# Performance work log

Hardware: AMD Instinct MI355X
Metric: run time of the kernel (lower is better)

## Reference

```python
import jax, jax.numpy as jnp
import numpy as np

DILATIONS = (1, 3, 5)
NUM_HEADS = 2


def _conv(x, w, b, dil=1, pad=0):
    # x: [B,C,H,W], w: [O,I,kh,kw] (OIHW), 'same'-style padding = dilation for k=3
    y = jax.lax.conv_general_dilated(
        x, w, window_strides=(1, 1), padding=[(pad, pad), (pad, pad)],
        rhs_dilation=(dil, dil), dimension_numbers=('NCHW', 'OIHW', 'NCHW'))
    return y + b[None, :, None, None]


def setup_inputs() -> dict:
    key = jax.random.key(0)
    ks = jax.random.split(key, 4)
    B, Cin, H, W = 4, 256, 64, 64
    Cout = 256
    x = jax.random.normal(ks[0], (B, Cin, H, W), dtype=jnp.float32)
    # kaiming-uniform-like init scale
    q_w = jax.random.uniform(ks[1], (Cout, Cin, 3, 3), dtype=jnp.float32,
                             minval=-1.0, maxval=1.0) * np.sqrt(6.0 / (Cin * 9))
    k_w = jax.random.uniform(ks[2], (Cout, Cin, 1, 1), dtype=jnp.float32,
                             minval=-1.0, maxval=1.0) * np.sqrt(6.0 / Cin)
    v_w = jax.random.uniform(ks[3], (Cout, Cin, 1, 1), dtype=jnp.float32,
                             minval=-1.0, maxval=1.0) * np.sqrt(6.0 / Cin)
    q_b = jnp.zeros((Cout,), jnp.float32)
    k_b = jnp.zeros((Cout,), jnp.float32)
    v_b = jnp.zeros((Cout,), jnp.float32)
    return {"x": x, "q_w": q_w, "q_b": q_b, "k_w": k_w, "k_b": k_b,
            "v_w": v_w, "v_b": v_b}


def reference(x, q_w, q_b, k_w, k_b, v_w, v_b):
    B, C, H, W = x.shape
    Cout = q_w.shape[0]
    hd = Cout // NUM_HEADS  # head_dim
    # ds_conv2d: sum of SiLU(dilated conv) over dilations 1,3,5 (padding=dilation)
    q = sum(jax.nn.silu(_conv(x, q_w, q_b, dil=d, pad=d)) for d in DILATIONS)
    k = _conv(x, k_w, k_b)
    v = _conv(x, v_w, v_b)
    N = H * W
    # [B, heads, head_dim, N]
    q = q.reshape(B, NUM_HEADS, hd, N)
    k = k.reshape(B, NUM_HEADS, hd, N)
    v = v.reshape(B, NUM_HEADS, hd, N)
    # energy[b,h,n,m] = sum_d q[b,h,d,n] * k[b,h,d,m]
    energy = jnp.einsum('bhdn,bhdm->bhnm', q, k)
    attn = jax.nn.softmax(energy / jnp.sqrt(jnp.float32(hd)), axis=-1)
    # out[b,h,n,d] = sum_m attn[b,h,n,m] * v[b,h,d,m]; then back to [B,C,H,W]
    out = jnp.einsum('bhnm,bhdm->bhdn', attn, v)
    return out.reshape(B, Cout, H, W)
```

## Files before the change

### kernel.cpp

```cpp
#include <hip/hip_runtime.h>
#include <cstdint>

typedef __attribute__((ext_vector_type(8))) _Float16 f16x8;
typedef __attribute__((ext_vector_type(4))) float f32x4;

#define DEV static __device__ __forceinline__

DEV void gld_lds16(void* lds_base, const void* gsrc) {
  __builtin_amdgcn_global_load_lds(
      (const __attribute__((address_space(1))) unsigned int*)gsrc,
      (__attribute__((address_space(3))) unsigned int*)lds_base,
      16, 0, 0);
}
DEV unsigned short f2h(float f) {
  _Float16 h = (_Float16)f;
  return __builtin_bit_cast(unsigned short, h);
}
DEV float h2f(unsigned short u) {
  _Float16 h = __builtin_bit_cast(_Float16, u);
  return (float)h;
}
DEV unsigned pk2h(float a, float b) {
  auto h2 = __builtin_amdgcn_cvt_pkrtz(a, b);
  return __builtin_bit_cast(unsigned, h2);
}
DEV float v_exp2(float x) { float r; asm("v_exp_f32 %0, %1" : "=v"(r) : "v"(x)); return r; }
DEV float v_rcp(float x) { float r; asm("v_rcp_f32 %0, %1" : "=v"(r) : "v"(x)); return r; }


__global__ __launch_bounds__(256) void k_prep_x(
    const float* __restrict__ x, char* __restrict__ xpad,
    const float* __restrict__ qw, const float* __restrict__ kw, const float* __restrict__ vw,
    unsigned short* __restrict__ Wq, unsigned short* __restrict__ Wk, unsigned short* __restrict__ Wv) {
  __shared__ float xs[32 * 257];
  int h = blockIdx.x, b = blockIdx.y, t = threadIdx.x;
  int gid = (b * 64 + h) * 256 + t;
  const float* q9 = qw + (size_t)gid * 9;
#pragma unroll
  for (int tp = 0; tp < 9; tp++) Wq[tp * 65536 + gid] = f2h(q9[tp]);
  Wk[gid] = f2h(kw[gid]);
  Wv[gid] = f2h(vw[gid]);
  uint4 z = {0, 0, 0, 0};
  char* rowbase = xpad + ((size_t)(b * 74 + h + 5) * 74) * 512;
  for (int i = t; i < 320; i += 256) {
    int col = i >> 5, off = (i & 31) * 16;
    int w = (col < 5) ? col : 64 + col;
    *(uint4*)(rowbase + (size_t)w * 512 + off) = z;
  }
  if (h < 10) {
    int r = (h < 5) ? h : 64 + h;
    char* rb = xpad + ((size_t)(b * 74 + r) * 74) * 512;
    for (int i = t; i < 2368; i += 256) *(uint4*)(rb + (size_t)i * 16) = z;
  }
  const float* xb = x + (size_t)b * 1048576 + h * 64;
  for (int half = 0; half < 2; half++) {
    int w0 = half * 32;
    for (int kk = 0; kk < 32; kk++) {
      int flat = kk * 256 + t;
      int ci = flat >> 5, w = flat & 31;
      xs[w * 257 + ci] = xb[ci * 4096 + w0 + w];
    }
    __syncthreads();
    for (int g = 0; g < 4; g++) {
      int w = g * 8 + (t >> 5);
      int cg = t & 31;
      float v0 = xs[w * 257 + cg * 8 + 0], v1 = xs[w * 257 + cg * 8 + 1];
      float v2 = xs[w * 257 + cg * 8 + 2], v3 = xs[w * 257 + cg * 8 + 3];
      float v4 = xs[w * 257 + cg * 8 + 4], v5 = xs[w * 257 + cg * 8 + 5];
      float v6 = xs[w * 257 + cg * 8 + 6], v7 = xs[w * 257 + cg * 8 + 7];
      uint4 pk;
      pk.x = pk2h(v0, v1);
      pk.y = pk2h(v2, v3);
      pk.z = pk2h(v4, v5);
      pk.w = pk2h(v6, v7);
      *(uint4*)(xpad + ((size_t)((b * 74 + h + 5) * 74) + w0 + w + 5) * 512 + cg * 16) = pk;
    }
    __syncthreads();
  }
}

__global__ __launch_bounds__(256, 2) void k_conv_kv(
    const char* __restrict__ xpad, const unsigned short* __restrict__ Wk,
    const unsigned short* __restrict__ Wv, const float* __restrict__ kb,
    const float* __restrict__ vb, unsigned short* __restrict__ K, unsigned short* __restrict__ V) {
  __shared__ char sm[65536];
  int t = threadIdx.x, lane = t & 63, wid = t >> 6, q4 = lane >> 4, l15 = lane & 15;
  int px0 = blockIdx.x * 128;
  int b = px0 >> 12, nn = px0 & 4095;
  int h = blockIdx.y;
  int mode = blockIdx.z;
  int co0 = h * 128;
  const char* Wsrc = (const char*)(mode ? Wv : Wk);
  int wm = wid & 1, wn = wid >> 1;

#define STAGE_KV(base_, c_)                                                       \
  {                                                                               \
    for (int ch = wid * 1024; ch < 16384; ch += 4096) {                           \
      int o = ch + lane * 16;                                                     \
      int r = o >> 7;                                                             \
      int n = nn + r, hh = n >> 6, ww2 = n & 63;                                  \
      int col = (o & 127) ^ ((r & 7) << 4);                                       \
      gld_lds16((base_) + ch,                                                     \
                xpad + ((size_t)((b * 74 + hh + 5) * 74) + ww2 + 5) * 512 + (c_)*128 + col); \
    }                                                                             \
    for (int ch = wid * 1024; ch < 16384; ch += 4096) {                           \
      int o = ch + lane * 16;                                                     \
      int r = o >> 7;                                                             \
      int col = (o & 127) ^ ((r & 7) << 4);                                       \
      gld_lds16((base_) + 16384 + ch, Wsrc + (co0 + r) * 512 + (c_)*128 + col);   \
    }                                                                             \
  }

  STAGE_KV(sm, 0);
  asm volatile("s_waitcnt vmcnt(0)" ::: "memory");
  __syncthreads();

  f32x4 acc[4][4] = {};
  for (int c = 0; c < 4; c++) {
    char* cb = sm + (c & 1) * 32768;
    if (c < 3) STAGE_KV(sm + ((c & 1) ^ 1) * 32768, c + 1);
    const char* Xs = cb;
    const char* Ws = cb + 16384;
    int xg = mode ? wn : wm;
    int wg = mode ? wm : wn;
#pragma unroll
    for (int kt = 0; kt < 2; kt++) {
      f16x8 xf[4], wf[4];
#pragma unroll
      for (int i = 0; i < 4; i++) {
        int rx = xg * 64 + i * 16 + l15;
        xf[i] = *(const f16x8*)(Xs + ((rx * 128 + kt * 64 + q4 * 16) ^ ((rx & 7) << 4)));
        int rw = wg * 64 + i * 16 + l15;
        wf[i] = *(const f16x8*)(Ws + ((rw * 128 + kt * 64 + q4 * 16) ^ ((rw & 7) << 4)));
      }
#pragma unroll
      for (int m = 0; m < 4; m++)
#pragma unroll
        for (int n = 0; n < 4; n++)
          acc[m][n] = mode ? __builtin_amdgcn_mfma_f32_16x16x32_f16(wf[m], xf[n], acc[m][n], 0, 0, 0)
                           : __builtin_amdgcn_mfma_f32_16x16x32_f16(xf[m], wf[n], acc[m][n], 0, 0, 0);
    }
    asm volatile("s_waitcnt vmcnt(0)" ::: "memory");
    __syncthreads();
  }
#undef STAGE_KV
  int bh = b * 2 + h;
  if (mode == 0) {
#pragma unroll
    for (int m = 0; m < 4; m++)
#pragma unroll
      for (int n = 0; n < 4; n++) {
        int dd = wn * 64 + n * 16 + l15;
        float bias = kb[co0 + dd];
#pragma unroll
        for (int j = 0; j < 4; j++) {
          int npix = nn + wm * 64 + m * 16 + q4 * 4 + j;
          K[(size_t)(bh * 4096 + npix) * 128 + dd] = f2h(acc[m][n][j] + bias);
        }
      }
  } else {
#pragma unroll
    for (int m = 0; m < 4; m++)
#pragma unroll
      for (int j = 0; j < 4; j++) {
        int cr = wm * 64 + m * 16 + q4 * 4 + j;
        float bias = vb[co0 + cr];
#pragma unroll
        for (int n = 0; n < 4; n++) {
          int pc = nn + wn * 64 + (n >> 1) * 32 + (l15 >> 2) * 8 + (n & 1) * 4 + (l15 & 3);
          V[(size_t)(bh * 128 + cr) * 4096 + pc] = f2h(acc[m][n][j] + bias);
        }
      }
  }
}

__global__ __launch_bounds__(512, 2) void k_conv_q(
    const char* __restrict__ xpad, const unsigned short* __restrict__ Wq,
    const float* __restrict__ qb, unsigned short* __restrict__ Q) {
  extern __shared__ char sm[];
  int t = threadIdx.x, lane = t & 63, wid = t >> 6, q4 = lane >> 4, l15 = lane & 15;
  int fblk = blockIdx.x;
  int g = (fblk & 7) * 32 + (fblk >> 3);
  int h2 = g & 31, b = (g >> 5) & 3, ch2 = g >> 7;
  int h0 = h2 * 2;
  int co0 = ch2 * 128;
  int wn = wid & 1, wq = wid >> 1;
  int hr = wq >> 1, wloc = wq & 1;
  const int dil[3] = {1, 3, 5};
  const char* WqB = (const char*)Wq;
  f32x4 accd[3][2][4] = {};

#define STAGE_B(dstbuf, kh_, c_, kw_)                                             \
  {                                                                               \
    const char* src_ = WqB + (size_t)((kh_)*3 + (kw_)) * 131072 + co0 * 512 + (c_)*128; \
    char* dst_ = (dstbuf);                                                        \
    for (int ch = wid * 1024; ch < 16384; ch += 8192) {                           \
      int o = ch + lane * 16;                                                     \
      int r = o >> 7;                                                             \
      int col = (o & 127) ^ ((r & 7) << 4);                                       \
      gld_lds16(dst_ + ch, src_ + r * 512 + col);                                 \
    }                                                                             \
  }

#define STAGE_A_ROW(abase_, slot_, pr_, c_)                                       \
  {                                                                               \
    const char* src_ = xpad + ((size_t)(b * 74 + (pr_)) * 74) * 512 + (c_)*128;   \
    char* dst_ = (abase_) + (slot_)*9472;                                         \
    for (int ch = wid * 1024; ch < 9472; ch += 8192) {                            \
      int o = ch + lane * 16;                                                     \
      if (o < 9472) {                                                             \
        int r = o >> 7;                                                           \
        int col = (o & 127) ^ ((r & 7) << 4);                                     \
        gld_lds16(dst_ + ch, src_ + r * 512 + col);                               \
      }                                                                           \
    }                                                                             \
  }

#define STAGE_A(abase_, kh_, c_)                                                  \
  {                                                                               \
    if ((kh_) == 1) {                                                             \
      for (int s = 0; s < 2; s++) STAGE_A_ROW(abase_, s, h0 + s + 5, c_);         \
    } else {                                                                      \
      for (int di = 0; di < 3; di++)                                              \
        for (int s = 0; s < 2; s++)                                               \
          STAGE_A_ROW(abase_, di * 2 + s, h0 + s + ((kh_)-1) * dil[di] + 5, c_);  \
    }                                                                             \
  }

  STAGE_A(sm + 32768, 0, 0);
  STAGE_B(sm, 0, 0, 0);
  asm volatile("s_waitcnt vmcnt(0)" ::: "memory");
  __syncthreads();

  int curB = 0, curA = 0;
  for (int kh = 0; kh < 3; kh++) {
    for (int c = 0; c < 4; c++) {
      int cn2 = c + 1, khn2 = kh;
      if (cn2 == 4) { cn2 = 0; khn2 = kh + 1; }
      for (int kw = 0; kw < 3; kw++) {
        int kwn = kw + 1, cn = c, khn = kh;
        if (kwn == 3) { kwn = 0; cn = c + 1; if (cn == 4) { cn = 0; khn = kh + 1; } }
        char* Bnext = curB ? sm : sm + 16384;
        if (khn < 3) STAGE_B(Bnext, khn, cn, kwn);
        if (kw == 0 && khn2 < 3) STAGE_A(sm + 32768 + (curA ^ 1) * 56832, khn2, cn2);
        const char* Bc = curB ? sm + 16384 : sm;
        const char* Abase = sm + 32768 + curA * 56832;
        f16x8 bf[4][2];
#pragma unroll
        for (int n = 0; n < 4; n++)
#pragma unroll
          for (int kt = 0; kt < 2; kt++) {
            int rc = wn * 64 + n * 16 + l15;
            bf[n][kt] = *(const f16x8*)(Bc + ((rc * 128 + kt * 64 + q4 * 16) ^ ((rc & 7) << 4)));
          }
#pragma unroll
        for (int di = 0; di < 3; di++) {
          int dw = (kw - 1) * dil[di] + 5;
          const char* Ad = Abase + (kh == 1 ? hr : di * 2 + hr) * 9472;
          f16x8 af[2][2];
#pragma unroll
          for (int m = 0; m < 2; m++)
#pragma unroll
            for (int kt = 0; kt < 2; kt++) {
              int wp = wloc * 32 + m * 16 + l15 + dw;
              af[m][kt] = *(const f16x8*)(Ad + ((wp * 128 + kt * 64 + q4 * 16) ^ ((wp & 7) << 4)));
            }
          __builtin_amdgcn_s_setprio(1);
#pragma unroll
          for (int m = 0; m < 2; m++)
#pragma unroll
            for (int n = 0; n < 4; n++)
#pragma unroll
              for (int kt = 0; kt < 2; kt++)
                accd[di][m][n] = __builtin_amdgcn_mfma_f32_16x16x32_f16(af[m][kt], bf[n][kt], accd[di][m][n], 0, 0, 0);
          __builtin_amdgcn_s_setprio(0);
        }
        asm volatile("s_waitcnt vmcnt(0)" ::: "memory");
        __syncthreads();
        curB ^= 1;
      }
      if (khn2 < 3) curA ^= 1;
    }
  }
#undef STAGE_A
#undef STAGE_A_ROW
#undef STAGE_B
  const float LOG2E = 1.4426950408889634f;
  const float QSCALE = 0.12751879523176862f;
#pragma unroll
  for (int n = 0; n < 4; n++) {
    float bias = qb[co0 + wn * 64 + n * 16 + l15];
#pragma unroll
    for (int m = 0; m < 2; m++)
#pragma unroll
      for (int j = 0; j < 4; j++) {
        float s = 0.f;
#pragma unroll
        for (int di = 0; di < 3; di++) {
          float v = accd[di][m][n][j] + bias;
          s += v * v_rcp(1.0f + v_exp2(-v * LOG2E));
        }
        int w = wloc * 32 + m * 16 + q4 * 4 + j;
        int npix = (h0 + hr) * 64 + w;
        int dd = wn * 64 + n * 16 + l15;
        Q[((size_t)(b * 2 + ch2) * 4096 + npix) * 128 + dd] = f2h(s * QSCALE);
      }
  }
}

__global__ __launch_bounds__(256, 2) void k_attn(
    const unsigned short* __restrict__ Q, const unsigned short* __restrict__ K,
    const unsigned short* __restrict__ V, float* __restrict__ out,
    unsigned short* __restrict__ o1buf, float* __restrict__ mlbuf) {
  __shared__ char sm[65536];
  int t = threadIdx.x, lane = t & 63, wid = t >> 6, q4 = lane >> 4, l15 = lane & 15;
  int fblk = blockIdx.x;
  int g = (fblk & 7) * 64 + (fblk >> 3);
  int nb = g & 31, bh = (g >> 5) & 7, half = g >> 8;
  int b = bh >> 1, hh = bh & 1;
  int n0 = nb * 128;
  const char* Qg = (const char*)(Q + ((size_t)bh * 4096 + n0) * 128);
  const char* Kg = (const char*)(K + (size_t)bh * 4096 * 128) + half * 524288;
  const char* Vg = (const char*)(V + (size_t)bh * 128 * 4096) + half * 4096;
  f16x8 qf[2][4];
#pragma unroll
  for (int nt = 0; nt < 2; nt++)
#pragma unroll
    for (int kt = 0; kt < 4; kt++) {
      int rn = wid * 32 + nt * 16 + l15;
      qf[nt][kt] = *(const f16x8*)(Qg + (size_t)rn * 256 + kt * 64 + q4 * 16);
    }
  const char* pT0 = sm + (((l15 * 256 + 0 * 64 + q4 * 16) ^ (l15 << 4)));
  const char* pT1 = sm + (((l15 * 256 + 1 * 64 + q4 * 16) ^ (l15 << 4)));
  const char* pT2 = sm + (((l15 * 256 + 2 * 64 + q4 * 16) ^ (l15 << 4)));
  const char* pT3 = sm + (((l15 * 256 + 3 * 64 + q4 * 16) ^ (l15 << 4)));
  const char* pU0 = sm + 32768 + (((l15 * 128 + 0 * 64 + q4 * 16) ^ ((l15 & 7) << 4)));
  const char* pU1 = sm + 32768 + (((l15 * 128 + 1 * 64 + q4 * 16) ^ ((l15 & 7) << 4)));
  int ks[4], vs[4], lch[4];
#pragma unroll
  for (int c2 = 0; c2 < 4; c2++) {
    int ch = wid * 1024 + c2 * 4096;
    int o = ch + lane * 16;
    lch[c2] = ch;
    ks[c2] = o ^ (((o >> 8) & 15) << 4);
    int dd = o >> 7;
    vs[c2] = dd * 8192 + ((o & 127) ^ ((dd & 7) << 4));
  }
#pragma unroll
  for (int c2 = 0; c2 < 4; c2++) gld_lds16(sm + lch[c2], Kg + ks[c2]);
#pragma unroll
  for (int c2 = 0; c2 < 4; c2++) gld_lds16(sm + 32768 + lch[c2], Vg + vs[c2]);
  asm volatile("s_waitcnt vmcnt(0)" ::: "memory");
  __syncthreads();
  f32x4 Ofr[8][2] = {};
  float mrun[2] = {-3e38f, -3e38f};
  float lrun[2] = {0.f, 0.f};
  const char* kgp = Kg;
  const char* vgp = Vg;

#define ATTN_ITER(KB, VB, KBN, VBN, do_pf)                                          \
  {                                                                                 \
    if (do_pf) {                                                                    \
      kgp += 16384;                                                                 \
      vgp += 128;                                                                   \
      _Pragma("unroll") for (int c2 = 0; c2 < 4; c2++)                              \
          gld_lds16(sm + (KBN) + lch[c2], kgp + ks[c2]);                            \
      _Pragma("unroll") for (int c2 = 0; c2 < 4; c2++)                              \
          gld_lds16(sm + (VBN) + lch[c2], vgp + vs[c2]);                            \
    }                                                                               \
    f32x4 sT[4][2] = {};                                                            \
    _Pragma("unroll") for (int kt = 0; kt < 4; kt++) {                              \
      const char* pT = (kt == 0) ? pT0 : (kt == 1) ? pT1 : (kt == 2) ? pT2 : pT3;   \
      f16x8 kf[4];                                                                  \
      _Pragma("unroll") for (int mt = 0; mt < 4; mt++)                              \
          kf[mt] = *(const f16x8*)(pT + (KB) + mt * 4096);                          \
      __builtin_amdgcn_s_setprio(1);                                                \
      _Pragma("unroll") for (int mt = 0; mt < 4; mt++)                              \
          _Pragma("unroll") for (int nt = 0; nt < 2; nt++)                          \
              sT[mt][nt] = __builtin_amdgcn_mfma_f32_16x16x32_f16(                  \
                  kf[mt], qf[nt][kt], sT[mt][nt], 0, 0, 0);                         \
      __builtin_amdgcn_s_setprio(0);                                                \
    }                                                                               \
    unsigned U[2][4][2];                                                            \
    _Pragma("unroll") for (int nt = 0; nt < 2; nt++) {                              \
      float mx = sT[0][nt][0];                                                      \
      _Pragma("unroll") for (int mt = 0; mt < 4; mt++)                              \
          _Pragma("unroll") for (int j = 0; j < 4; j++) mx = fmaxf(mx, sT[mt][nt][j]); \
      mx = fmaxf(mx, __shfl_xor(mx, 16));                                           \
      mx = fmaxf(mx, __shfl_xor(mx, 32));                                           \
      float mn = mrun[nt];                                                          \
      if (!__all(mx - mn <= 8.f)) {                                                 \
        mn = fmaxf(mrun[nt], mx);                                                   \
        float al = v_exp2(mrun[nt] - mn);                                           \
        mrun[nt] = mn;                                                              \
        lrun[nt] *= al;                                                             \
        _Pragma("unroll") for (int dt = 0; dt < 8; dt++) Ofr[dt][nt] *= al;         \
      }                                                                             \
      float rs = 0.f;                                                               \
      _Pragma("unroll") for (int mt = 0; mt < 4; mt++) {                            \
        float p0 = v_exp2(sT[mt][nt][0] - mn);                                      \
        float p1 = v_exp2(sT[mt][nt][1] - mn);                                      \
        float p2 = v_exp2(sT[mt][nt][2] - mn);                                      \
        float p3 = v_exp2(sT[mt][nt][3] - mn);                                      \
        rs += (p0 + p1) + (p2 + p3);                                                \
        U[nt][mt][0] = pk2h(p0, p1);                                                \
        U[nt][mt][1] = pk2h(p2, p3);                                                \
      }                                                                             \
      rs += __shfl_xor(rs, 16);                                                     \
      rs += __shfl_xor(rs, 32);                                                     \
      lrun[nt] += rs;                                                               \
    }                                                                               \
    _Pragma("unroll") for (int kt = 0; kt < 2; kt++) {                              \
      const char* pU = kt ? pU1 : pU0;                                              \
      f16x8 pf[2];                                                                  \
      _Pragma("unroll") for (int nt = 0; nt < 2; nt++) {                            \
        uint4 fr;                                                                   \
        fr.x = U[nt][2 * kt][0];                                                    \
        fr.y = U[nt][2 * kt][1];                                                    \
        fr.z = U[nt][2 * kt + 1][0];                                                \
        fr.w = U[nt][2 * kt + 1][1];                                                \
        pf[nt] = __builtin_bit_cast(f16x8, fr);                                     \
      }                                                                             \
      f16x8 vf[8];                                                                  \
      _Pragma("unroll") for (int dt = 0; dt < 8; dt++)                              \
          vf[dt] = *(const f16x8*)(pU + ((VB)-32768) + dt * 2048);                  \
      __builtin_amdgcn_s_setprio(1);                                                \
      _Pragma("unroll") for (int dt = 0; dt < 8; dt++)                              \
          _Pragma("unroll") for (int nt = 0; nt < 2; nt++)                          \
              Ofr[dt][nt] = __builtin_amdgcn_mfma_f32_16x16x32_f16(                 \
                  vf[dt], pf[nt], Ofr[dt][nt], 0, 0, 0);                            \
      __builtin_amdgcn_s_setprio(0);                                                \
    }                                                                               \
    __syncthreads();                                                                \
  }

  for (int it2 = 0; it2 < 16; it2++) {
    ATTN_ITER(0, 32768, 16384, 49152, true);
    ATTN_ITER(16384, 49152, 0, 32768, (it2 < 15));
  }
#undef ATTN_ITER

  if (q4 == 0) {
#pragma unroll
    for (int nt = 0; nt < 2; nt++) {
      int n = n0 + wid * 32 + nt * 16 + l15;
      float2 ml;
      ml.x = mrun[nt];
      ml.y = lrun[nt];
      *(float2*)(mlbuf + ((size_t)(half * 8 + bh) * 4096 + n) * 2) = ml;
    }
  }
  if (half == 0) {
    float* og = out + (size_t)(b * 256 + hh * 128) * 4096 + n0 + wid * 32;
#pragma unroll
    for (int dt = 0; dt < 8; dt++)
#pragma unroll
      for (int nt = 0; nt < 2; nt++)
#pragma unroll
        for (int j = 0; j < 4; j++) {
          int dd = dt * 16 + q4 * 4 + j;
          og[(size_t)dd * 4096 + nt * 16 + l15] = Ofr[dt][nt][j];
        }
  } else {
    float li[2] = {v_rcp(lrun[0]), v_rcp(lrun[1])};
    unsigned short* og = o1buf + (size_t)bh * 128 * 4096 + n0 + wid * 32;
#pragma unroll
    for (int dt = 0; dt < 8; dt++)
#pragma unroll
      for (int nt = 0; nt < 2; nt++)
#pragma unroll
        for (int j = 0; j < 4; j++) {
          int dd = dt * 16 + q4 * 4 + j;
          og[(size_t)dd * 4096 + nt * 16 + l15] = f2h(Ofr[dt][nt][j] * li[nt]);
        }
  }
}

__global__ __launch_bounds__(256) void k_combine(
    float* __restrict__ out, const unsigned short* __restrict__ o1,
    const float* __restrict__ ml) {
  int tid = blockIdx.x * 256 + threadIdx.x;
  int n = tid & 4095, dg = (tid >> 12) & 7, bh = tid >> 15;
  float2 ml0 = *(const float2*)(ml + ((size_t)bh * 4096 + n) * 2);
  float2 ml1 = *(const float2*)(ml + ((size_t)(8 + bh) * 4096 + n) * 2);
  float ms = fmaxf(ml0.x, ml1.x);
  float a0 = v_exp2(ml0.x - ms);
  float w1 = ml1.y * v_exp2(ml1.x - ms);
  float inv = 1.f / (ml0.y * a0 + w1);
  size_t ob = ((size_t)((bh >> 1) * 256 + (bh & 1) * 128 + dg * 16)) * 4096 + n;
  size_t o1b = ((size_t)(bh * 128 + dg * 16)) * 4096 + n;
#pragma unroll 4
  for (int j = 0; j < 16; j++) {
    float v0 = out[ob + (size_t)j * 4096];
    float v1 = h2f(o1[o1b + (size_t)j * 4096]);
    out[ob + (size_t)j * 4096] = (v0 * a0 + v1 * w1) * inv;
  }
}

extern "C" void kernel_launch(void* const* d_in, const int* in_sizes, int n_in,
                              void* d_out, int out_size, void* d_ws, size_t ws_size,
                              hipStream_t stream) {
  (void)in_sizes; (void)n_in; (void)out_size;
  const float* x  = (const float*)d_in[0];
  const float* qw = (const float*)d_in[1];
  const float* qb = (const float*)d_in[2];
  const float* kw = (const float*)d_in[3];
  const float* kb = (const float*)d_in[4];
  const float* vw = (const float*)d_in[5];
  const float* vb = (const float*)d_in[6];
  char* ws = (char*)d_ws;
  if (ws_size < 37822464) return;
  char* xpad = ws;
  unsigned short* Wq = (unsigned short*)(ws + 11214848);
  unsigned short* Wk = (unsigned short*)(ws + 12394496);
  unsigned short* Wv = (unsigned short*)(ws + 12525568);
  unsigned short* Qb = (unsigned short*)(ws + 12656640);
  unsigned short* Kb = (unsigned short*)(ws + 21045248);
  unsigned short* Vb = (unsigned short*)(ws + 29433856);
  unsigned short* O1 = (unsigned short*)ws;
  float* ML = (float*)(ws + 11214848);
  k_prep_x<<<dim3(64, 4), dim3(256), 0, stream>>>(x, xpad, qw, kw, vw, Wq, Wk, Wv);
  k_conv_kv<<<dim3(128, 2, 2), dim3(256), 0, stream>>>(xpad, Wk, Wv, kb, vb, Kb, Vb);
  k_conv_q<<<dim3(256), dim3(512), 146432, stream>>>(xpad, Wq, qb, Qb);
  k_attn<<<dim3(512), dim3(256), 0, stream>>>(Qb, Kb, Vb, (float*)d_out, O1, ML);
  k_combine<<<dim3(1024), dim3(256), 0, stream>>>((float*)d_out, O1, ML);
}
```

Baseline: 164.2 us.

## Merge split-KV halves into one block and combine partial softmax in LDS

The attention kernel now runs both KV halves as two 256-thread groups inside one 512-thread block, each with its own 64KB LDS region. Group 1 passes its unnormalized accumulators and running max/sum to group 0 through LDS, and group 0 merges them and writes the final output. This removes the separate combine kernel, the fp16 partial-output and max/sum buffers, and the extra read-modify-write of the fp32 output in global memory. In exchange it uses 128KB of dynamic LDS per block, adds a block-wide barrier plus an LDS exchange at the end, and leaves half the threads idle during the final store.

```diff
diff --git a/kernel.cpp b/kernel.cpp
--- a/kernel.cpp
+++ b/kernel.cpp
@@ -15,10 +15,6 @@
 DEV unsigned short f2h(float f) {
   _Float16 h = (_Float16)f;
   return __builtin_bit_cast(unsigned short, h);
-}
-DEV float h2f(unsigned short u) {
-  _Float16 h = __builtin_bit_cast(_Float16, u);
-  return (float)h;
 }
 DEV unsigned pk2h(float a, float b) {
   auto h2 = __builtin_amdgcn_cvt_pkrtz(a, b);
@@ -308,17 +304,18 @@
   }
 }
 
-__global__ __launch_bounds__(256, 2) void k_attn(
+__global__ __launch_bounds__(512) void k_attn(
     const unsigned short* __restrict__ Q, const unsigned short* __restrict__ K,
-    const unsigned short* __restrict__ V, float* __restrict__ out,
-    unsigned short* __restrict__ o1buf, float* __restrict__ mlbuf) {
-  __shared__ char sm[65536];
+    const unsigned short* __restrict__ V, float* __restrict__ out) {
+  extern __shared__ char sm[];
   int t = threadIdx.x, lane = t & 63, wid = t >> 6, q4 = lane >> 4, l15 = lane & 15;
+  int half = wid >> 2, wv = wid & 3;
   int fblk = blockIdx.x;
-  int g = (fblk & 7) * 64 + (fblk >> 3);
-  int nb = g & 31, bh = (g >> 5) & 7, half = g >> 8;
+  int g = (fblk & 7) * 32 + (fblk >> 3);
+  int nb = g & 31, bh = g >> 5;
   int b = bh >> 1, hh = bh & 1;
   int n0 = nb * 128;
+  char* smg = sm + half * 65536;
   const char* Qg = (const char*)(Q + ((size_t)bh * 4096 + n0) * 128);
   const char* Kg = (const char*)(K + (size_t)bh * 4096 * 128) + half * 524288;
   const char* Vg = (const char*)(V + (size_t)bh * 128 * 4096) + half * 4096;
@@ -327,19 +324,19 @@
   for (int nt = 0; nt < 2; nt++)
 #pragma unroll
     for (int kt = 0; kt < 4; kt++) {
-      int rn = wid * 32 + nt * 16 + l15;
+      int rn = wv * 32 + nt * 16 + l15;
       qf[nt][kt] = *(const f16x8*)(Qg + (size_t)rn * 256 + kt * 64 + q4 * 16);
     }
-  const char* pT0 = sm + (((l15 * 256 + 0 * 64 + q4 * 16) ^ (l15 << 4)));
-  const char* pT1 = sm + (((l15 * 256 + 1 * 64 + q4 * 16) ^ (l15 << 4)));
-  const char* pT2 = sm + (((l15 * 256 + 2 * 64 + q4 * 16) ^ (l15 << 4)));
-  const char* pT3 = sm + (((l15 * 256 + 3 * 64 + q4 * 16) ^ (l15 << 4)));
-  const char* pU0 = sm + 32768 + (((l15 * 128 + 0 * 64 + q4 * 16) ^ ((l15 & 7) << 4)));
-  const char* pU1 = sm + 32768 + (((l15 * 128 + 1 * 64 + q4 * 16) ^ ((l15 & 7) << 4)));
+  const char* pT0 = smg + (((l15 * 256 + 0 * 64 + q4 * 16) ^ (l15 << 4)));
+  const char* pT1 = smg + (((l15 * 256 + 1 * 64 + q4 * 16) ^ (l15 << 4)));
+  const char* pT2 = smg + (((l15 * 256 + 2 * 64 + q4 * 16) ^ (l15 << 4)));
+  const char* pT3 = smg + (((l15 * 256 + 3 * 64 + q4 * 16) ^ (l15 << 4)));
+  const char* pU0 = smg + 32768 + (((l15 * 128 + 0 * 64 + q4 * 16) ^ ((l15 & 7) << 4)));
+  const char* pU1 = smg + 32768 + (((l15 * 128 + 1 * 64 + q4 * 16) ^ ((l15 & 7) << 4)));
   int ks[4], vs[4], lch[4];
 #pragma unroll
   for (int c2 = 0; c2 < 4; c2++) {
-    int ch = wid * 1024 + c2 * 4096;
+    int ch = wv * 1024 + c2 * 4096;
     int o = ch + lane * 16;
     lch[c2] = ch;
     ks[c2] = o ^ (((o >> 8) & 15) << 4);
@@ -347,9 +344,9 @@
     vs[c2] = dd * 8192 + ((o & 127) ^ ((dd & 7) << 4));
   }
 #pragma unroll
-  for (int c2 = 0; c2 < 4; c2++) gld_lds16(sm + lch[c2], Kg + ks[c2]);
-#pragma unroll
-  for (int c2 = 0; c2 < 4; c2++) gld_lds16(sm + 32768 + lch[c2], Vg + vs[c2]);
+  for (int c2 = 0; c2 < 4; c2++) gld_lds16(smg + lch[c2], Kg + ks[c2]);
+#pragma unroll
+  for (int c2 = 0; c2 < 4; c2++) gld_lds16(smg + 32768 + lch[c2], Vg + vs[c2]);
   asm volatile("s_waitcnt vmcnt(0)" ::: "memory");
   __syncthreads();
   f32x4 Ofr[8][2] = {};
@@ -364,9 +361,9 @@
       kgp += 16384;                                                                 \
       vgp += 128;                                                                   \
       _Pragma("unroll") for (int c2 = 0; c2 < 4; c2++)                              \
-          gld_lds16(sm + (KBN) + lch[c2], kgp + ks[c2]);                            \
+          gld_lds16(smg + (KBN) + lch[c2], kgp + ks[c2]);                           \
       _Pragma("unroll") for (int c2 = 0; c2 < 4; c2++)                              \
-          gld_lds16(sm + (VBN) + lch[c2], vgp + vs[c2]);                            \
+          gld_lds16(smg + (VBN) + lch[c2], vgp + vs[c2]);                           \
     }                                                                               \
     f32x4 sT[4][2] = {};                                                            \
     _Pragma("unroll") for (int kt = 0; kt < 4; kt++) {                              \
@@ -440,18 +437,35 @@
   }
 #undef ATTN_ITER
 
-  if (q4 == 0) {
+  float* xch = (float*)sm;
+  float* mlx = (float*)(sm + 65536);
+  int slot = t & 255;
+  if (half == 1) {
+#pragma unroll
+    for (int dt = 0; dt < 8; dt++)
+#pragma unroll
+      for (int nt = 0; nt < 2; nt++)
+#pragma unroll
+        for (int j = 0; j < 4; j++)
+          xch[(dt * 8 + nt * 4 + j) * 256 + slot] = Ofr[dt][nt][j];
+    mlx[slot] = mrun[0];
+    mlx[256 + slot] = mrun[1];
+    mlx[512 + slot] = lrun[0];
+    mlx[768 + slot] = lrun[1];
+  }
+  __syncthreads();
+  if (half == 0) {
+    float m1[2] = {mlx[slot], mlx[256 + slot]};
+    float l1[2] = {mlx[512 + slot], mlx[768 + slot]};
+    float a0[2], a1[2], li[2];
 #pragma unroll
     for (int nt = 0; nt < 2; nt++) {
-      int n = n0 + wid * 32 + nt * 16 + l15;
-      float2 ml;
-      ml.x = mrun[nt];
-      ml.y = lrun[nt];
-      *(float2*)(mlbuf + ((size_t)(half * 8 + bh) * 4096 + n) * 2) = ml;
+      float ms = fmaxf(mrun[nt], m1[nt]);
+      a0[nt] = v_exp2(mrun[nt] - ms);
+      a1[nt] = v_exp2(m1[nt] - ms);
+      li[nt] = v_rcp(lrun[nt] * a0[nt] + l1[nt] * a1[nt]);
     }
-  }
-  if (half == 0) {
-    float* og = out + (size_t)(b * 256 + hh * 128) * 4096 + n0 + wid * 32;
+    float* og = out + (size_t)(b * 256 + hh * 128) * 4096 + n0 + wv * 32;
 #pragma unroll
     for (int dt = 0; dt < 8; dt++)
 #pragma unroll
@@ -459,41 +473,10 @@
 #pragma unroll
         for (int j = 0; j < 4; j++) {
           int dd = dt * 16 + q4 * 4 + j;
-          og[(size_t)dd * 4096 + nt * 16 + l15] = Ofr[dt][nt][j];
+          float o1v = xch[(dt * 8 + nt * 4 + j) * 256 + slot];
+          og[(size_t)dd * 4096 + nt * 16 + l15] =
+              (Ofr[dt][nt][j] * a0[nt] + o1v * a1[nt]) * li[nt];
         }
-  } else {
-    float li[2] = {v_rcp(lrun[0]), v_rcp(lrun[1])};
-    unsigned short* og = o1buf + (size_t)bh * 128 * 4096 + n0 + wid * 32;
-#pragma unroll
-    for (int dt = 0; dt < 8; dt++)
-#pragma unroll
-      for (int nt = 0; nt < 2; nt++)
-#pragma unroll
-        for (int j = 0; j < 4; j++) {
-          int dd = dt * 16 + q4 * 4 + j;
-          og[(size_t)dd * 4096 + nt * 16 + l15] = f2h(Ofr[dt][nt][j] * li[nt]);
-        }
-  }
-}
-
-__global__ __launch_bounds__(256) void k_combine(
-    float* __restrict__ out, const unsigned short* __restrict__ o1,
-    const float* __restrict__ ml) {
-  int tid = blockIdx.x * 256 + threadIdx.x;
-  int n = tid & 4095, dg = (tid >> 12) & 7, bh = tid >> 15;
-  float2 ml0 = *(const float2*)(ml + ((size_t)bh * 4096 + n) * 2);
-  float2 ml1 = *(const float2*)(ml + ((size_t)(8 + bh) * 4096 + n) * 2);
-  float ms = fmaxf(ml0.x, ml1.x);
-  float a0 = v_exp2(ml0.x - ms);
-  float w1 = ml1.y * v_exp2(ml1.x - ms);
-  float inv = 1.f / (ml0.y * a0 + w1);
-  size_t ob = ((size_t)((bh >> 1) * 256 + (bh & 1) * 128 + dg * 16)) * 4096 + n;
-  size_t o1b = ((size_t)(bh * 128 + dg * 16)) * 4096 + n;
-#pragma unroll 4
-  for (int j = 0; j < 16; j++) {
-    float v0 = out[ob + (size_t)j * 4096];
-    float v1 = h2f(o1[o1b + (size_t)j * 4096]);
-    out[ob + (size_t)j * 4096] = (v0 * a0 + v1 * w1) * inv;
   }
 }
 
@@ -517,11 +500,8 @@
   unsigned short* Qb = (unsigned short*)(ws + 12656640);
   unsigned short* Kb = (unsigned short*)(ws + 21045248);
   unsigned short* Vb = (unsigned short*)(ws + 29433856);
-  unsigned short* O1 = (unsigned short*)ws;
-  float* ML = (float*)(ws + 11214848);
   k_prep_x<<<dim3(64, 4), dim3(256), 0, stream>>>(x, xpad, qw, kw, vw, Wq, Wk, Wv);
   k_conv_kv<<<dim3(128, 2, 2), dim3(256), 0, stream>>>(xpad, Wk, Wv, kb, vb, Kb, Vb);
   k_conv_q<<<dim3(256), dim3(512), 146432, stream>>>(xpad, Wq, qb, Qb);
-  k_attn<<<dim3(512), dim3(256), 0, stream>>>(Qb, Kb, Vb, (float*)d_out, O1, ML);
-  k_combine<<<dim3(1024), dim3(256), 0, stream>>>((float*)d_out, O1, ML);
-}
+  k_attn<<<dim3(256), dim3(512), 131072, stream>>>(Qb, Kb, Vb, (float*)d_out);
+}
```

Result: faster. 155.4 us (-5.4%).
